# Kernel tuning notes

Hardware: AMD Instinct MI355X
Metric: run time of the kernel (lower is better)

## Reference

```python
import jax, jax.numpy as jnp
import numpy as np

B, S, D, H, HD = 1, 2048, 3072, 24, 128
FFN = int(D / 3 * 8)  # 8192
ADALN = 256
NORM_EPS = 1e-6
QK_EPS = 1e-5
AXES_DIMS = (16, 56, 56)
AXES_LENS = (64, 128, 128)
THETA = 256.0


def rmsnorm(x, w, eps):
    var = jnp.mean(jnp.square(x), axis=-1, keepdims=True)
    return x * jax.lax.rsqrt(var + eps) * w


def apply_rope(x, cos, sin):
    # x: [B,S,H,HD]; cos/sin: [B,S,HD//2] (broadcast over heads, matching freqs_cis.unsqueeze(2))
    xr = x[..., 0::2]
    xi = x[..., 1::2]
    c = cos[:, :, None, :]
    s = sin[:, :, None, :]
    or_ = xr * c - xi * s
    oi_ = xr * s + xi * c
    return jnp.stack([or_, oi_], axis=-1).reshape(x.shape)


def rope_angles(ids):
    # ids: [B,S,3] int; returns angles [B,S,HD//2] concatenated per axis like RopeEmbedder
    parts = []
    for d, idx_axis in zip(AXES_DIMS, range(len(AXES_DIMS))):
        freqs = 1.0 / (THETA ** (jnp.arange(0, d, 2, dtype=jnp.float32) / d))  # [d/2]
        ang = ids[..., idx_axis].astype(jnp.float32)[..., None] * freqs  # [B,S,d/2]
        parts.append(ang)
    return jnp.concatenate(parts, axis=-1)  # [B,S,64]


def setup_inputs() -> dict:
    key = jax.random.key(0)
    ks = jax.random.split(key, 20)
    w = 0.02
    ids = jnp.concatenate([
        jax.random.randint(ks[15], (B, S, 1), 0, AXES_LENS[0]),
        jax.random.randint(ks[16], (B, S, 1), 0, AXES_LENS[1]),
        jax.random.randint(ks[17], (B, S, 1), 0, AXES_LENS[2]),
    ], axis=-1)
    return {
        "x": jax.random.normal(ks[0], (B, S, D), jnp.float32),
        "adaln_input": jax.random.normal(ks[1], (B, ADALN), jnp.float32),
        "attn_mask": jnp.ones((B, S), dtype=bool),
        "ids": ids,
        "attn_norm1_w": jnp.ones((D,), jnp.float32),
        "attn_norm2_w": jnp.ones((D,), jnp.float32),
        "ffn_norm1_w": jnp.ones((D,), jnp.float32),
        "ffn_norm2_w": jnp.ones((D,), jnp.float32),
        "norm_q_w": jnp.ones((HD,), jnp.float32),
        "norm_k_w": jnp.ones((HD,), jnp.float32),
        "wq": jax.random.normal(ks[2], (D, D), jnp.float32) * w,
        "wk": jax.random.normal(ks[3], (D, D), jnp.float32) * w,
        "wv": jax.random.normal(ks[4], (D, D), jnp.float32) * w,
        "wo": jax.random.normal(ks[5], (D, D), jnp.float32) * w,
        "w1": jax.random.normal(ks[6], (D, FFN), jnp.float32) * w,
        "w2": jax.random.normal(ks[7], (FFN, D), jnp.float32) * w,
        "w3": jax.random.normal(ks[8], (D, FFN), jnp.float32) * w,
        "adaln_w": jax.random.normal(ks[9], (ADALN, 4 * D), jnp.float32) * w,
        "adaln_b": jnp.zeros((4 * D,), jnp.float32),
    }


def block_forward(x, adaln_input, attn_mask, ids,
                  attn_norm1_w, attn_norm2_w, ffn_norm1_w, ffn_norm2_w,
                  norm_q_w, norm_k_w, wq, wk, wv, wo, w1, w2, w3,
                  adaln_w, adaln_b):
    ang = rope_angles(ids)
    cos, sin = jnp.cos(ang), jnp.sin(ang)

    mod = adaln_input @ adaln_w + adaln_b
    scale_msa, gate_msa, scale_mlp, gate_mlp = jnp.split(mod[:, None, :], 4, axis=2)
    gate_msa, gate_mlp = jnp.tanh(gate_msa), jnp.tanh(gate_mlp)
    scale_msa, scale_mlp = 1.0 + scale_msa, 1.0 + scale_mlp

    # Attention branch
    xs = rmsnorm(x, attn_norm1_w, NORM_EPS) * scale_msa  # [B,S,D]
    q = (xs @ wq).reshape(B, S, H, HD)
    k = (xs @ wk).reshape(B, S, H, HD)
    v = (xs @ wv).reshape(B, S, H, HD)
    q = rmsnorm(q, norm_q_w, QK_EPS)
    k = rmsnorm(k, norm_k_w, QK_EPS)
    q = apply_rope(q, cos, sin)
    k = apply_rope(k, cos, sin)

    scores = jnp.einsum('bqhd,bkhd->bhqk', q, k) / jnp.sqrt(jnp.float32(HD))
    neg = jnp.finfo(scores.dtype).min
    scores = jnp.where(attn_mask[:, None, None, :], scores, neg)
    probs = jax.nn.softmax(scores, axis=-1)
    attn = jnp.einsum('bhqk,bkhd->bqhd', probs, v).reshape(B, S, D)
    attn_out = attn @ wo

    x = x + gate_msa * rmsnorm(attn_out, attn_norm2_w, NORM_EPS)

    # FFN branch (SwiGLU)
    xf = rmsnorm(x, ffn_norm1_w, NORM_EPS) * scale_mlp
    h = jax.nn.silu(xf @ w1) * (xf @ w3)
    ffn_out = h @ w2
    x = x + gate_mlp * rmsnorm(ffn_out, ffn_norm2_w, NORM_EPS)
    return x


def reference(x, adaln_input, attn_mask, ids,
              attn_norm1_w, attn_norm2_w, ffn_norm1_w, ffn_norm2_w,
              norm_q_w, norm_k_w, wq, wk, wv, wo, w1, w2, w3,
              adaln_w, adaln_b):
    return block_forward(x, adaln_input, attn_mask, ids,
                         attn_norm1_w, attn_norm2_w, ffn_norm1_w, ffn_norm2_w,
                         norm_q_w, norm_k_w, wq, wk, wv, wo, w1, w2, w3,
                         adaln_w, adaln_b)
```

## Files before the change

### kernel.cpp

```cpp
#include <hip/hip_runtime.h>

#define AS1 __attribute__((address_space(1)))
#define AS3 __attribute__((address_space(3)))

typedef __bf16 bf16;
using bf16x8 = __attribute__((ext_vector_type(8))) __bf16;
using bf16x4 = __attribute__((ext_vector_type(4))) __bf16;
using bf16x2 = __attribute__((ext_vector_type(2))) __bf16;
using f32x4  = __attribute__((ext_vector_type(4))) float;


__device__ inline float wsum(float v) {
#pragma unroll
  for (int o = 32; o; o >>= 1) v += __shfl_xor(v, o, 64);
  return v;
}

template <int EPI>
__global__ __launch_bounds__(512, 1) void gemm256(
    const bf16* __restrict__ A, const bf16* __restrict__ Bt, void* __restrict__ Cv,
    int K, int lda, int ldb, int ldc, long long kOff, long long sC) {
  __shared__ bf16 lds[2][2][256 * 64];
  const int t = threadIdx.x;
  const int lane = t & 63, wid = t >> 6;
  const int wm = wid >> 2, wn = wid & 3;
  const int row16 = lane & 15, kg = lane >> 4;
  const int m0 = blockIdx.x * 256, n0 = blockIdx.y * 256;
  const int NT = K >> 6;
  const int sgran = (lane & 7) ^ (lane >> 3);
  A += (long long)blockIdx.z * kOff;
  Bt += (long long)blockIdx.z * kOff;

  auto stageA = [&](int buf, int r, int tk) {
    const int wrow = ((wid & 4) << 5) + (r << 5) + ((wid & 3) << 3);
    __builtin_amdgcn_global_load_lds(
        (const AS1 void*)(A + (long long)(m0 + wrow + (lane >> 3)) * lda + tk * 64 +
                          (sgran << 3)),
        (AS3 void*)&lds[buf][0][wrow * 64], 16, 0, 0);
  };
  auto stageB = [&](int buf, int r, int tk) {
    const int wrow = ((wid & 4) << 5) + (r << 5) + ((wid & 3) << 3);
    __builtin_amdgcn_global_load_lds(
        (const AS1 void*)(Bt + (long long)(n0 + wrow + (lane >> 3)) * ldb + tk * 64 +
                          (sgran << 3)),
        (AS3 void*)&lds[buf][1][wrow * 64], 16, 0, 0);
  };

  f32x4 acc[8][4];
#pragma unroll
  for (int i = 0; i < 8; ++i)
#pragma unroll
    for (int j = 0; j < 4; ++j) acc[i][j] = (f32x4){0.f, 0.f, 0.f, 0.f};

#pragma unroll
  for (int r = 0; r < 4; ++r) { stageA(0, r, 0); stageB(0, r, 0); }
#pragma unroll
  for (int r = 0; r < 3; ++r) { stageA(1, r, 1); stageB(1, r, 1); }

  bf16x8 bfr[4][2], af[2][2];

  for (int kt = 0; kt < NT; ++kt) {
    const int cb = kt & 1, nb = cb ^ 1;
    if (kt + 1 < NT) asm volatile("s_waitcnt vmcnt(6)" ::: "memory");
    else             asm volatile("s_waitcnt vmcnt(0)" ::: "memory");
    __builtin_amdgcn_s_barrier();

    if (kt + 1 < NT) { stageA(nb, 3, kt + 1); stageB(nb, 3, kt + 1); }
#pragma unroll
    for (int ni = 0; ni < 4; ++ni)
#pragma unroll
      for (int kk = 0; kk < 2; ++kk) {
        const int r = wn * 64 + ni * 16 + row16;
        bfr[ni][kk] = *(const bf16x8*)&lds[cb][1][r * 64 + (((kk * 4 + kg) ^ (r & 7)) << 3)];
      }
#pragma unroll
    for (int mi = 0; mi < 2; ++mi)
#pragma unroll
      for (int kk = 0; kk < 2; ++kk) {
        const int r = wm * 128 + mi * 16 + row16;
        af[mi][kk] = *(const bf16x8*)&lds[cb][0][r * 64 + (((kk * 4 + kg) ^ (r & 7)) << 3)];
      }
    __builtin_amdgcn_s_barrier();
    asm volatile("s_waitcnt lgkmcnt(0)" ::: "memory");
    __builtin_amdgcn_s_setprio(1);
#pragma unroll
    for (int kk = 0; kk < 2; ++kk)
#pragma unroll
      for (int mi = 0; mi < 2; ++mi)
#pragma unroll
        for (int ni = 0; ni < 4; ++ni)
          acc[mi][ni] =
              __builtin_amdgcn_mfma_f32_16x16x32_bf16(af[mi][kk], bfr[ni][kk], acc[mi][ni], 0, 0, 0);
    __builtin_amdgcn_s_setprio(0);

#pragma unroll
    for (int q = 1; q < 4; ++q) {
      __builtin_amdgcn_s_barrier();
      if (kt + 2 < NT) { stageA(cb, q - 1, kt + 2); stageB(cb, q - 1, kt + 2); }
#pragma unroll
      for (int mi = 0; mi < 2; ++mi)
#pragma unroll
        for (int kk = 0; kk < 2; ++kk) {
          const int r = wm * 128 + q * 32 + mi * 16 + row16;
          af[mi][kk] = *(const bf16x8*)&lds[cb][0][r * 64 + (((kk * 4 + kg) ^ (r & 7)) << 3)];
        }
      __builtin_amdgcn_s_barrier();
      asm volatile("s_waitcnt lgkmcnt(0)" ::: "memory");
      __builtin_amdgcn_s_setprio(1);
#pragma unroll
      for (int kk = 0; kk < 2; ++kk)
#pragma unroll
        for (int mi = 0; mi < 2; ++mi)
#pragma unroll
          for (int ni = 0; ni < 4; ++ni)
            acc[q * 2 + mi][ni] = __builtin_amdgcn_mfma_f32_16x16x32_bf16(
                af[mi][kk], bfr[ni][kk], acc[q * 2 + mi][ni], 0, 0, 0);
      __builtin_amdgcn_s_setprio(0);
    }
  }

  float* Cf = (float*)Cv;
  bf16* Cb = (bf16*)Cv;
  const long long cz = (long long)blockIdx.z * sC;
#pragma unroll
  for (int mf = 0; mf < 8; ++mf)
#pragma unroll
    for (int ni = 0; ni < 4; ++ni)
#pragma unroll
      for (int rr = 0; rr < 4; ++rr) {
        const int row = m0 + wm * 128 + (mf >> 1) * 32 + (mf & 1) * 16 + kg * 4 + rr;
        const int col = n0 + wn * 64 + ni * 16 + row16;
        const long long idx = cz + (long long)row * ldc + col;
        const float v = acc[mf][ni][rr];
        if constexpr (EPI == 0) Cf[idx] = v;
        else Cb[idx] = (bf16)v;
      }
}

__global__ __launch_bounds__(256) void flash_attn_k(const bf16* __restrict__ qkv,
                                                    const bf16* __restrict__ vt,
                                                    float* __restrict__ Op,
                                                    float* __restrict__ mlp) {
  __shared__ bf16 Ks[64 * 128];
  __shared__ bf16 Vs[128 * 64];
  __shared__ bf16 Ps[4 * 32 * 64];
  const int t = threadIdx.x, lane = t & 63, wid = t >> 6;
  const int row16 = lane & 15, kg = lane >> 4;
  const int q0 = blockIdx.x * 128;
  const int h = blockIdx.y;
  const int z = blockIdx.z;
  const bf16* Qp = qkv + h * 128;
  const bf16* Kp = qkv + 3072 + h * 128;
  const bf16* Vt = vt + (long long)h * 262144;
  const float iscale = 0.08838834764831845f;

  bf16x8 qf[2][4];
#pragma unroll
  for (int mi = 0; mi < 2; ++mi)
#pragma unroll
    for (int kc = 0; kc < 4; ++kc)
      qf[mi][kc] = *(const bf16x8*)&Qp[(long long)(q0 + wid * 32 + mi * 16 + row16) * 9216 +
                                       kc * 32 + kg * 8];
  bf16x8 ones;
#pragma unroll
  for (int j = 0; j < 8; ++j) ones[j] = (bf16)1.0f;

  f32x4 oacc[2][8];
#pragma unroll
  for (int mi = 0; mi < 2; ++mi)
#pragma unroll
    for (int nd = 0; nd < 8; ++nd) oacc[mi][nd] = (f32x4){0.f, 0.f, 0.f, 0.f};
  f32x4 lacc[2] = {(f32x4){0.f, 0.f, 0.f, 0.f}, (f32x4){0.f, 0.f, 0.f, 0.f}};
  float mst[2][4];
#pragma unroll
  for (int mi = 0; mi < 2; ++mi)
#pragma unroll
    for (int r = 0; r < 4; ++r) mst[mi][r] = -1e30f;

  bf16* Pw = &Ps[wid * 2048];
  const int kvbase = z << 10;

  for (int kv0 = kvbase; kv0 < kvbase + 1024; kv0 += 64) {
#pragma unroll
    for (int p = 0; p < 4; ++p) {
      const int gi = p * 256 + t;
      const int row = gi >> 4, g = gi & 15;
      __builtin_amdgcn_global_load_lds(
          (const AS1 void*)(Kp + (long long)(kv0 + row) * 9216 + ((g ^ (row & 7)) << 3)),
          (AS3 void*)&Ks[(p * 256 + wid * 64) * 8], 16, 0, 0);
    }
#pragma unroll
    for (int p = 0; p < 4; ++p) {
      const int gi = p * 256 + t;
      const int row = gi >> 3, g = gi & 7;
      __builtin_amdgcn_global_load_lds(
          (const AS1 void*)(Vt + (long long)row * 2048 + kv0 + ((g ^ (row & 7)) << 3)),
          (AS3 void*)&Vs[(p * 256 + wid * 64) * 8], 16, 0, 0);
    }
    __syncthreads();

    f32x4 sacc[2][4];
#pragma unroll
    for (int mi = 0; mi < 2; ++mi)
#pragma unroll
      for (int nf = 0; nf < 4; ++nf) sacc[mi][nf] = (f32x4){0.f, 0.f, 0.f, 0.f};
#pragma unroll
    for (int kc = 0; kc < 4; ++kc) {
      bf16x8 kf[4];
#pragma unroll
      for (int nf = 0; nf < 4; ++nf) {
        const int row = nf * 16 + row16;
        kf[nf] = *(const bf16x8*)&Ks[(row * 16 + ((kc * 4 + kg) ^ (row & 7))) * 8];
      }
#pragma unroll
      for (int mi = 0; mi < 2; ++mi)
#pragma unroll
        for (int nf = 0; nf < 4; ++nf)
          sacc[mi][nf] =
              __builtin_amdgcn_mfma_f32_16x16x32_bf16(qf[mi][kc], kf[nf], sacc[mi][nf], 0, 0, 0);
    }

    float fac[2][4];
#pragma unroll
    for (int mi = 0; mi < 2; ++mi)
#pragma unroll
      for (int r = 0; r < 4; ++r) {
        float rm = sacc[mi][0][r];
#pragma unroll
        for (int nf = 1; nf < 4; ++nf) rm = fmaxf(rm, sacc[mi][nf][r]);
        rm = fmaxf(rm, __shfl_xor(rm, 1, 64));
        rm = fmaxf(rm, __shfl_xor(rm, 2, 64));
        rm = fmaxf(rm, __shfl_xor(rm, 4, 64));
        rm = fmaxf(rm, __shfl_xor(rm, 8, 64));
        const float mnew = fmaxf(mst[mi][r], rm * iscale);
        fac[mi][r] = __expf(mst[mi][r] - mnew);
        mst[mi][r] = mnew;
#pragma unroll
        for (int nf = 0; nf < 4; ++nf)
          sacc[mi][nf][r] = __expf(sacc[mi][nf][r] * iscale - mnew);
      }
#pragma unroll
    for (int mi = 0; mi < 2; ++mi)
#pragma unroll
      for (int r = 0; r < 4; ++r) {
        lacc[mi][r] *= fac[mi][r];
#pragma unroll
        for (int nd = 0; nd < 8; ++nd) oacc[mi][nd][r] *= fac[mi][r];
      }

#pragma unroll
    for (int mi = 0; mi < 2; ++mi)
#pragma unroll
      for (int nf = 0; nf < 4; ++nf)
#pragma unroll
        for (int r = 0; r < 4; ++r) {
          const int row = mi * 16 + kg * 4 + r;
          const int col = nf * 16 + row16;
          Pw[(row * 8 + ((col >> 3) ^ (row & 7))) * 8 + (col & 7)] = (bf16)sacc[mi][nf][r];
        }

#pragma unroll
    for (int kvc = 0; kvc < 2; ++kvc) {
      bf16x8 pf[2], vf[8];
#pragma unroll
      for (int mi = 0; mi < 2; ++mi) {
        const int row = mi * 16 + row16;
        pf[mi] = *(const bf16x8*)&Pw[(row * 8 + ((kvc * 4 + kg) ^ (row & 7))) * 8];
      }
#pragma unroll
      for (int nd = 0; nd < 8; ++nd) {
        const int row = nd * 16 + row16;
        vf[nd] = *(const bf16x8*)&Vs[(row * 8 + ((kvc * 4 + kg) ^ (row & 7))) * 8];
      }
#pragma unroll
      for (int mi = 0; mi < 2; ++mi) {
        lacc[mi] = __builtin_amdgcn_mfma_f32_16x16x32_bf16(pf[mi], ones, lacc[mi], 0, 0, 0);
#pragma unroll
        for (int nd = 0; nd < 8; ++nd)
          oacc[mi][nd] =
              __builtin_amdgcn_mfma_f32_16x16x32_bf16(pf[mi], vf[nd], oacc[mi][nd], 0, 0, 0);
      }
    }
    __syncthreads();
  }

  float* Oz = Op + (long long)z * 6291456;
#pragma unroll
  for (int mi = 0; mi < 2; ++mi)
#pragma unroll
    for (int nd = 0; nd < 8; ++nd)
#pragma unroll
      for (int r = 0; r < 4; ++r) {
        const int row = q0 + wid * 32 + mi * 16 + kg * 4 + r;
        const int col = h * 128 + nd * 16 + row16;
        Oz[(long long)row * 3072 + col] = oacc[mi][nd][r];
      }
  if (row16 == 0) {
#pragma unroll
    for (int mi = 0; mi < 2; ++mi)
#pragma unroll
      for (int r = 0; r < 4; ++r) {
        const int s = q0 + wid * 32 + mi * 16 + kg * 4 + r;
        const long long mi2 = ((long long)z * 49152 + s * 24 + h) * 2;
        mlp[mi2] = mst[mi][r];
        mlp[mi2 + 1] = lacc[mi][r];
      }
  }
}

__global__ __launch_bounds__(256) void fa_combine_k(const float* __restrict__ Op,
                                                    const float* __restrict__ mlp,
                                                    bf16* __restrict__ attn) {
  const int t = threadIdx.x, lane = t & 63, wid = t >> 6;
  const int pair = blockIdx.x * 4 + wid;
  const int s = pair / 24, h = pair % 24;
  const float2 ml0 = *(const float2*)&mlp[(long long)pair * 2];
  const float2 ml1 = *(const float2*)&mlp[(49152LL + pair) * 2];
  const float m = fmaxf(ml0.x, ml1.x);
  const float a0 = __expf(ml0.x - m), a1 = __expf(ml1.x - m);
  const float inv = 1.f / (ml0.y * a0 + ml1.y * a1);
  const long long base = (long long)s * 3072 + h * 128 + lane * 2;
  const float2 o0 = *(const float2*)&Op[base];
  const float2 o1 = *(const float2*)&Op[6291456LL + base];
  bf16x2 o;
  o[0] = (bf16)((o0.x * a0 + o1.x * a1) * inv);
  o[1] = (bf16)((o0.y * a0 + o1.y * a1) * inv);
  *(bf16x2*)&attn[base] = o;
}

__device__ inline void convT_tile(const float* __restrict__ in, bf16* __restrict__ out,
                                  int R, int C, int bx, int by) {
  __shared__ float tile[64][65];
  const int t = threadIdx.x;
  const int r0 = by * 64, c0 = bx * 64;
#pragma unroll
  for (int it = 0; it < 4; ++it) {
    const int idx = it * 256 + t;
    const int rl = idx >> 4, c4 = (idx & 15) << 2;
    const float4 v = *(const float4*)&in[(long long)(r0 + rl) * C + c0 + c4];
    tile[rl][c4 + 0] = v.x;
    tile[rl][c4 + 1] = v.y;
    tile[rl][c4 + 2] = v.z;
    tile[rl][c4 + 3] = v.w;
  }
  __syncthreads();
#pragma unroll
  for (int it = 0; it < 4; ++it) {
    const int idx = it * 256 + t;
    const int cl = idx >> 4, r4 = (idx & 15) << 2;
    bf16x4 o;
    o[0] = (bf16)tile[r4 + 0][cl];
    o[1] = (bf16)tile[r4 + 1][cl];
    o[2] = (bf16)tile[r4 + 2][cl];
    o[3] = (bf16)tile[r4 + 3][cl];
    *(bf16x4*)&out[(long long)(c0 + cl) * R + r0 + r4] = o;
  }
}

__global__ __launch_bounds__(256) void convAll(
    const float* __restrict__ wq, const float* __restrict__ wk,
    const float* __restrict__ wv, const float* __restrict__ wo,
    const float* __restrict__ w1, const float* __restrict__ w3,
    const float* __restrict__ w2, bf16* __restrict__ wqkvT, bf16* __restrict__ woT,
    bf16* __restrict__ w13T, bf16* __restrict__ w2T) {
  const int id = blockIdx.x;
  if (id < 9216) {
    const int m = id / 2304, l = id % 2304;
    const float* in = m == 0 ? wq : m == 1 ? wk : m == 2 ? wv : wo;
    bf16* out = m < 3 ? wqkvT + (long long)m * 9437184 : woT;
    convT_tile(in, out, 3072, 3072, l % 48, l / 48);
  } else if (id < 21504) {
    int l = id - 9216;
    const int m = l / 6144;
    l %= 6144;
    convT_tile(m ? w3 : w1, w13T + (long long)m * 25165824, 3072, 8192, l % 128, l / 128);
  } else {
    const int l = id - 21504;
    convT_tile(w2, w2T, 8192, 3072, l % 48, l / 48);
  }
}

__global__ __launch_bounds__(256) void ropetab_k(const int* __restrict__ ids,
                                                 float* __restrict__ cosT,
                                                 float* __restrict__ sinT) {
  const int i = blockIdx.x * 256 + threadIdx.x;
  const int s = i >> 6, j = i & 63;
  int ax, fi;
  float d;
  if (j < 8) { ax = 0; fi = j; d = 16.f; }
  else if (j < 36) { ax = 1; fi = j - 8; d = 56.f; }
  else { ax = 2; fi = j - 36; d = 56.f; }
  const float freq = exp2f(-16.f * (float)fi / d);
  const float ang = (float)ids[s * 3 + ax] * freq;
  cosT[i] = cosf(ang);
  sinT[i] = sinf(ang);
}

__global__ __launch_bounds__(256) void adaln_kernel(const float* __restrict__ ain,
                                                    const float* __restrict__ W,
                                                    const float* __restrict__ b,
                                                    float* __restrict__ out) {
  __shared__ float a[256];
  const int t = threadIdx.x;
  a[t] = ain[t];
  __syncthreads();
  const int n = blockIdx.x * 256 + t;
  float acc = b[n];
  for (int k = 0; k < 256; ++k) acc = fmaf(a[k], W[(long long)k * 12288 + n], acc);
  const int chunk = n / 3072;
  out[n] = (chunk & 1) ? tanhf(acc) : (1.f + acc);
}

__global__ __launch_bounds__(256) void rmsnorm_scale_k(const float* __restrict__ x,
                                                       const float* __restrict__ w,
                                                       const float* __restrict__ scale,
                                                       bf16* __restrict__ out) {
  __shared__ float red[4];
  const int t = threadIdx.x, lane = t & 63, wid = t >> 6;
  const long long base = (long long)blockIdx.x * 3072;
  float v[12];
  float ss = 0.f;
#pragma unroll
  for (int ch = 0; ch < 3; ++ch) {
    const float4 f = *(const float4*)&x[base + ch * 1024 + t * 4];
    v[ch * 4 + 0] = f.x; v[ch * 4 + 1] = f.y; v[ch * 4 + 2] = f.z; v[ch * 4 + 3] = f.w;
    ss += f.x * f.x + f.y * f.y + f.z * f.z + f.w * f.w;
  }
  ss = wsum(ss);
  if (!lane) red[wid] = ss;
  __syncthreads();
  const float r = rsqrtf((red[0] + red[1] + red[2] + red[3]) / 3072.f + 1e-6f);
#pragma unroll
  for (int ch = 0; ch < 3; ++ch) {
    const int col = ch * 1024 + t * 4;
    bf16x4 o;
#pragma unroll
    for (int j = 0; j < 4; ++j) o[j] = (bf16)(v[ch * 4 + j] * r * w[col + j] * scale[col + j]);
    *(bf16x4*)&out[base + col] = o;
  }
}

__global__ __launch_bounds__(256) void qknorm_rope_k(bf16* __restrict__ qkv,
                                                     const float* __restrict__ cosT,
                                                     const float* __restrict__ sinT,
                                                     const float* __restrict__ wq,
                                                     const float* __restrict__ wk) {
  const int t = threadIdx.x, lane = t & 63, wid = t >> 6;
  const int idx = blockIdx.x * 4 + wid;
  const int s = idx / 24, h = idx % 24;
  const int isK = blockIdx.y;
  bf16* base = qkv + (long long)s * 9216 + isK * 3072 + h * 128;
  bf16x2 p = *(const bf16x2*)(base + 2 * lane);
  float xr = (float)p[0], xi = (float)p[1];
  const float ss = wsum(xr * xr + xi * xi);
  const float r = rsqrtf(ss / 128.f + 1e-5f);
  const float* w = isK ? wk : wq;
  const float2 wv = *(const float2*)&w[2 * lane];
  xr *= r * wv.x;
  xi *= r * wv.y;
  const float c = cosT[s * 64 + lane], sn = sinT[s * 64 + lane];
  bf16x2 o;
  o[0] = (bf16)(xr * c - xi * sn);
  o[1] = (bf16)(xr * sn + xi * c);
  *(bf16x2*)(base + 2 * lane) = o;
}

__global__ __launch_bounds__(256) void vtrans_k(const bf16* __restrict__ qkv,
                                                bf16* __restrict__ vt) {
  __shared__ bf16 tile[64][72];
  const int t = threadIdx.x;
  const int s0 = blockIdx.x * 64, d0 = blockIdx.y * 64, h = blockIdx.z;
#pragma unroll
  for (int it = 0; it < 2; ++it) {
    const int idx = it * 256 + t;
    const int sl = idx >> 3, c8 = (idx & 7) << 3;
    const bf16x8 v =
        *(const bf16x8*)&qkv[(long long)(s0 + sl) * 9216 + 6144 + h * 128 + d0 + c8];
    *(bf16x8*)&tile[sl][c8] = v;
  }
  __syncthreads();
#pragma unroll
  for (int it = 0; it < 2; ++it) {
    const int idx = it * 256 + t;
    const int dl = idx >> 3, s8 = (idx & 7) << 3;
    bf16x8 o;
#pragma unroll
    for (int j = 0; j < 8; ++j) o[j] = tile[s8 + j][dl];
    *(bf16x8*)&vt[(long long)h * 262144 + (long long)(d0 + dl) * 2048 + s0 + s8] = o;
  }
}

__global__ __launch_bounds__(256) void silumul_k(const bf16* __restrict__ t13,
                                                 bf16* __restrict__ h) {
  const int gi = blockIdx.x * 256 + threadIdx.x;
  const int s = gi >> 10, j8 = (gi & 1023) << 3;
  const bf16x8 a = *(const bf16x8*)&t13[(long long)s * 16384 + j8];
  const bf16x8 b = *(const bf16x8*)&t13[(long long)s * 16384 + 8192 + j8];
  bf16x8 o;
#pragma unroll
  for (int j = 0; j < 8; ++j) {
    const float x = (float)a[j];
    const float sl = x / (1.f + __expf(-x));
    o[j] = (bf16)(sl * (float)b[j]);
  }
  *(bf16x8*)&h[(long long)s * 8192 + j8] = o;
}

__global__ __launch_bounds__(256) void resid1_k(
    const float* __restrict__ x, const float* __restrict__ p0, const float* __restrict__ p1,
    const float* __restrict__ n2w, const float* __restrict__ gate,
    const float* __restrict__ f1w, const float* __restrict__ smlp,
    float* __restrict__ x1, bf16* __restrict__ xf) {
  __shared__ float red[8];
  const int t = threadIdx.x, lane = t & 63, wid = t >> 6;
  const long long base = (long long)blockIdx.x * 3072;
  float av[12];
  float ss = 0.f;
#pragma unroll
  for (int ch = 0; ch < 3; ++ch) {
    const float4 f0 = *(const float4*)&p0[base + ch * 1024 + t * 4];
    const float4 f1 = *(const float4*)&p1[base + ch * 1024 + t * 4];
    const float a0 = f0.x + f1.x, a1 = f0.y + f1.y, a2 = f0.z + f1.z, a3 = f0.w + f1.w;
    av[ch * 4 + 0] = a0; av[ch * 4 + 1] = a1; av[ch * 4 + 2] = a2; av[ch * 4 + 3] = a3;
    ss += a0 * a0 + a1 * a1 + a2 * a2 + a3 * a3;
  }
  ss = wsum(ss);
  if (!lane) red[wid] = ss;
  __syncthreads();
  const float r = rsqrtf((red[0] + red[1] + red[2] + red[3]) / 3072.f + 1e-6f);
  float xv[12];
  float ss2 = 0.f;
#pragma unroll
  for (int ch = 0; ch < 3; ++ch) {
    const int col = ch * 1024 + t * 4;
    const float4 f = *(const float4*)&x[base + col];
    float4 o;
    o.x = f.x + gate[col + 0] * (av[ch * 4 + 0] * r * n2w[col + 0]);
    o.y = f.y + gate[col + 1] * (av[ch * 4 + 1] * r * n2w[col + 1]);
    o.z = f.z + gate[col + 2] * (av[ch * 4 + 2] * r * n2w[col + 2]);
    o.w = f.w + gate[col + 3] * (av[ch * 4 + 3] * r * n2w[col + 3]);
    *(float4*)&x1[base + col] = o;
    xv[ch * 4 + 0] = o.x; xv[ch * 4 + 1] = o.y; xv[ch * 4 + 2] = o.z; xv[ch * 4 + 3] = o.w;
    ss2 += o.x * o.x + o.y * o.y + o.z * o.z + o.w * o.w;
  }
  ss2 = wsum(ss2);
  if (!lane) red[4 + wid] = ss2;
  __syncthreads();
  const float r2 = rsqrtf((red[4] + red[5] + red[6] + red[7]) / 3072.f + 1e-6f);
#pragma unroll
  for (int ch = 0; ch < 3; ++ch) {
    const int col = ch * 1024 + t * 4;
    bf16x4 o;
#pragma unroll
    for (int j = 0; j < 4; ++j)
      o[j] = (bf16)(xv[ch * 4 + j] * r2 * f1w[col + j] * smlp[col + j]);
    *(bf16x4*)&xf[base + col] = o;
  }
}

__global__ __launch_bounds__(256) void resid2_k(const float* __restrict__ x1,
                                                const float* __restrict__ f0,
                                                const float* __restrict__ f1,
                                                const float* __restrict__ nw,
                                                const float* __restrict__ gate,
                                                float* __restrict__ out) {
  __shared__ float red[4];
  const int t = threadIdx.x, lane = t & 63, wid = t >> 6;
  const long long base = (long long)blockIdx.x * 3072;
  float fv[12];
  float ss = 0.f;
#pragma unroll
  for (int ch = 0; ch < 3; ++ch) {
    const float4 a = *(const float4*)&f0[base + ch * 1024 + t * 4];
    const float4 b = *(const float4*)&f1[base + ch * 1024 + t * 4];
    const float a0 = a.x + b.x, a1 = a.y + b.y, a2 = a.z + b.z, a3 = a.w + b.w;
    fv[ch * 4 + 0] = a0; fv[ch * 4 + 1] = a1; fv[ch * 4 + 2] = a2; fv[ch * 4 + 3] = a3;
    ss += a0 * a0 + a1 * a1 + a2 * a2 + a3 * a3;
  }
  ss = wsum(ss);
  if (!lane) red[wid] = ss;
  __syncthreads();
  const float r = rsqrtf((red[0] + red[1] + red[2] + red[3]) / 3072.f + 1e-6f);
#pragma unroll
  for (int ch = 0; ch < 3; ++ch) {
    const int col = ch * 1024 + t * 4;
    const float4 f = *(const float4*)&x1[base + col];
    float4 o;
    o.x = f.x + gate[col + 0] * (fv[ch * 4 + 0] * r * nw[col + 0]);
    o.y = f.y + gate[col + 1] * (fv[ch * 4 + 1] * r * nw[col + 1]);
    o.z = f.z + gate[col + 2] * (fv[ch * 4 + 2] * r * nw[col + 2]);
    o.w = f.w + gate[col + 3] * (fv[ch * 4 + 3] * r * nw[col + 3]);
    *(float4*)&out[base + col] = o;
  }
}

extern "C" void kernel_launch(void* const* d_in, const int* in_sizes, int n_in,
                              void* d_out, int out_size, void* d_ws, size_t ws_size,
                              hipStream_t stream) {
  const float* x    = (const float*)d_in[0];
  const float* ain  = (const float*)d_in[1];
  const int* ids    = (const int*)d_in[3];
  const float* n1w  = (const float*)d_in[4];
  const float* n2w  = (const float*)d_in[5];
  const float* fn1w = (const float*)d_in[6];
  const float* fn2w = (const float*)d_in[7];
  const float* nqw  = (const float*)d_in[8];
  const float* nkw  = (const float*)d_in[9];
  const float* wq   = (const float*)d_in[10];
  const float* wk   = (const float*)d_in[11];
  const float* wv   = (const float*)d_in[12];
  const float* wo   = (const float*)d_in[13];
  const float* w1   = (const float*)d_in[14];
  const float* w2   = (const float*)d_in[15];
  const float* w3   = (const float*)d_in[16];
  const float* adw  = (const float*)d_in[17];
  const float* adb  = (const float*)d_in[18];

  if (ws_size < 395362304ULL) return;

  char* ws = (char*)d_ws;
  bf16* wqkvT = (bf16*)(ws + 0LL);
  bf16* woT   = (bf16*)(ws + 56623104LL);
  bf16* w13T  = (bf16*)(ws + 75497472LL);
  bf16* w2T   = (bf16*)(ws + 176160768LL);
  float* cosT = (float*)(ws + 226492416LL);
  float* sinT = (float*)(ws + 227016704LL);
  float* adv  = (float*)(ws + 227540992LL);
  bf16* xs    = (bf16*)(ws + 227590144LL);
  char* big   = ws + 240173056LL;
  float* x1   = (float*)(big);
  bf16* qkv   = (bf16*)(big + 25165824LL);
  bf16* vt    = (bf16*)(big + 62914560LL);
  bf16* attn  = (bf16*)(big + 75497472LL);
  float* aoP  = (float*)(big + 88080384LL);
  float* Opart= (float*)(big + 88080384LL);
  float* mlp  = (float*)(big + 138412032LL);
  bf16* t13   = (bf16*)(big + 25165824LL);
  bf16* hbuf  = (bf16*)(big + 92274688LL);
  float* ffnP = (float*)(big + 25165824LL);

  const dim3 b256(256);
  const dim3 b512(512);

  ropetab_k<<<dim3(512), b256, 0, stream>>>(ids, cosT, sinT);
  adaln_kernel<<<dim3(48), b256, 0, stream>>>(ain, adw, adb, adv);

  convAll<<<dim3(27648), b256, 0, stream>>>(wq, wk, wv, wo, w1, w3, w2, wqkvT, woT, w13T,
                                            w2T);

  rmsnorm_scale_k<<<dim3(2048), b256, 0, stream>>>(x, n1w, adv, xs);

  gemm256<1><<<dim3(8, 36, 1), b512, 0, stream>>>(xs, wqkvT, qkv, 3072, 3072, 3072, 9216,
                                                  0LL, 0LL);

  qknorm_rope_k<<<dim3(12288, 2), b256, 0, stream>>>(qkv, cosT, sinT, nqw, nkw);
  vtrans_k<<<dim3(32, 2, 24), b256, 0, stream>>>(qkv, vt);

  flash_attn_k<<<dim3(16, 24, 2), b256, 0, stream>>>(qkv, vt, Opart, mlp);
  fa_combine_k<<<dim3(12288), b256, 0, stream>>>(Opart, mlp, attn);

  gemm256<0><<<dim3(8, 12, 2), b512, 0, stream>>>(attn, woT, aoP, 1536, 3072, 3072, 3072,
                                                  1536LL, 6291456LL);
  resid1_k<<<dim3(2048), b256, 0, stream>>>(x, aoP, aoP + 6291456LL, n2w, adv + 3072, fn1w,
                                            adv + 6144, x1, xs);
  gemm256<1><<<dim3(8, 64, 1), b512, 0, stream>>>(xs, w13T, t13, 3072, 3072, 3072, 16384,
                                                  0LL, 0LL);
  silumul_k<<<dim3(8192), b256, 0, stream>>>(t13, hbuf);
  gemm256<0><<<dim3(8, 12, 2), b512, 0, stream>>>(hbuf, w2T, ffnP, 4096, 8192, 8192, 3072,
                                                  4096LL, 6291456LL);
  resid2_k<<<dim3(2048), b256, 0, stream>>>(x1, ffnP, ffnP + 6291456LL, fn2w, adv + 9216,
                                            (float*)d_out);
}
```

Measured before the change: 886.1 us.

## Template GEMM on N-tile width and use 256x192 tiles for QKV, Wo, W2

Parameterizes the bf16 GEMM kernel on the number of 16-wide N fragments per wave, splitting LDS into separate A and B buffers and adapting the B staging pattern for 192-wide tiles. The QKV, output-projection and W2 GEMMs switch to 256x192 tiles so their grids (384 and 256 blocks) map onto the CU count better than the old 288- and 192-block grids with 256x256 tiles. The secondary barrier after each LDS fragment read is also removed to cut synchronization. The trade-off is lower arithmetic intensity per tile and more global traffic for B, plus some risk from the relaxed barrier schedule.

```diff
diff --git a/kernel.cpp b/kernel.cpp
--- a/kernel.cpp
+++ b/kernel.cpp
@@ -16,16 +16,19 @@
   return v;
 }
 
-template <int EPI>
+template <int EPI, int NI>
 __global__ __launch_bounds__(512, 1) void gemm256(
     const bf16* __restrict__ A, const bf16* __restrict__ Bt, void* __restrict__ Cv,
     int K, int lda, int ldb, int ldc, long long kOff, long long sC) {
-  __shared__ bf16 lds[2][2][256 * 64];
+  constexpr int BN = NI * 64;
+  constexpr int BROUNDS = (NI == 4) ? 4 : 3;
+  __shared__ bf16 ldsA[2][256 * 64];
+  __shared__ bf16 ldsB[2][BN * 64];
   const int t = threadIdx.x;
   const int lane = t & 63, wid = t >> 6;
   const int wm = wid >> 2, wn = wid & 3;
   const int row16 = lane & 15, kg = lane >> 4;
-  const int m0 = blockIdx.x * 256, n0 = blockIdx.y * 256;
+  const int m0 = blockIdx.x * 256, n0 = blockIdx.y * BN;
   const int NT = K >> 6;
   const int sgran = (lane & 7) ^ (lane >> 3);
   A += (long long)blockIdx.z * kOff;
@@ -36,28 +39,32 @@
     __builtin_amdgcn_global_load_lds(
         (const AS1 void*)(A + (long long)(m0 + wrow + (lane >> 3)) * lda + tk * 64 +
                           (sgran << 3)),
-        (AS3 void*)&lds[buf][0][wrow * 64], 16, 0, 0);
+        (AS3 void*)&ldsA[buf][wrow * 64], 16, 0, 0);
   };
   auto stageB = [&](int buf, int r, int tk) {
-    const int wrow = ((wid & 4) << 5) + (r << 5) + ((wid & 3) << 3);
+    int wrow;
+    if constexpr (NI == 4) wrow = ((wid & 4) << 5) + (r << 5) + ((wid & 3) << 3);
+    else                   wrow = r * 64 + wid * 8;
     __builtin_amdgcn_global_load_lds(
         (const AS1 void*)(Bt + (long long)(n0 + wrow + (lane >> 3)) * ldb + tk * 64 +
                           (sgran << 3)),
-        (AS3 void*)&lds[buf][1][wrow * 64], 16, 0, 0);
+        (AS3 void*)&ldsB[buf][wrow * 64], 16, 0, 0);
   };
 
-  f32x4 acc[8][4];
+  f32x4 acc[8][NI];
 #pragma unroll
   for (int i = 0; i < 8; ++i)
 #pragma unroll
-    for (int j = 0; j < 4; ++j) acc[i][j] = (f32x4){0.f, 0.f, 0.f, 0.f};
-
-#pragma unroll
-  for (int r = 0; r < 4; ++r) { stageA(0, r, 0); stageB(0, r, 0); }
+    for (int j = 0; j < NI; ++j) acc[i][j] = (f32x4){0.f, 0.f, 0.f, 0.f};
+
+#pragma unroll
+  for (int r = 0; r < 4; ++r) stageA(0, r, 0);
+#pragma unroll
+  for (int r = 0; r < BROUNDS; ++r) stageB(0, r, 0);
 #pragma unroll
   for (int r = 0; r < 3; ++r) { stageA(1, r, 1); stageB(1, r, 1); }
 
-  bf16x8 bfr[4][2], af[2][2];
+  bf16x8 bfr[NI][2], af[2][2];
 
   for (int kt = 0; kt < NT; ++kt) {
     const int cb = kt & 1, nb = cb ^ 1;
@@ -65,22 +72,24 @@
     else             asm volatile("s_waitcnt vmcnt(0)" ::: "memory");
     __builtin_amdgcn_s_barrier();
 
-    if (kt + 1 < NT) { stageA(nb, 3, kt + 1); stageB(nb, 3, kt + 1); }
-#pragma unroll
-    for (int ni = 0; ni < 4; ++ni)
+    if (kt + 1 < NT) {
+      stageA(nb, 3, kt + 1);
+      if constexpr (NI == 4) stageB(nb, 3, kt + 1);
+    }
+#pragma unroll
+    for (int ni = 0; ni < NI; ++ni)
 #pragma unroll
       for (int kk = 0; kk < 2; ++kk) {
-        const int r = wn * 64 + ni * 16 + row16;
-        bfr[ni][kk] = *(const bf16x8*)&lds[cb][1][r * 64 + (((kk * 4 + kg) ^ (r & 7)) << 3)];
+        const int r = wn * (16 * NI) + ni * 16 + row16;
+        bfr[ni][kk] = *(const bf16x8*)&ldsB[cb][r * 64 + (((kk * 4 + kg) ^ (r & 7)) << 3)];
       }
 #pragma unroll
     for (int mi = 0; mi < 2; ++mi)
 #pragma unroll
       for (int kk = 0; kk < 2; ++kk) {
         const int r = wm * 128 + mi * 16 + row16;
-        af[mi][kk] = *(const bf16x8*)&lds[cb][0][r * 64 + (((kk * 4 + kg) ^ (r & 7)) << 3)];
-      }
-    __builtin_amdgcn_s_barrier();
+        af[mi][kk] = *(const bf16x8*)&ldsA[cb][r * 64 + (((kk * 4 + kg) ^ (r & 7)) << 3)];
+      }
     asm volatile("s_waitcnt lgkmcnt(0)" ::: "memory");
     __builtin_amdgcn_s_setprio(1);
 #pragma unroll
@@ -88,7 +97,7 @@
 #pragma unroll
       for (int mi = 0; mi < 2; ++mi)
 #pragma unroll
-        for (int ni = 0; ni < 4; ++ni)
+        for (int ni = 0; ni < NI; ++ni)
           acc[mi][ni] =
               __builtin_amdgcn_mfma_f32_16x16x32_bf16(af[mi][kk], bfr[ni][kk], acc[mi][ni], 0, 0, 0);
     __builtin_amdgcn_s_setprio(0);
@@ -102,9 +111,8 @@
 #pragma unroll
         for (int kk = 0; kk < 2; ++kk) {
           const int r = wm * 128 + q * 32 + mi * 16 + row16;
-          af[mi][kk] = *(const bf16x8*)&lds[cb][0][r * 64 + (((kk * 4 + kg) ^ (r & 7)) << 3)];
+          af[mi][kk] = *(const bf16x8*)&ldsA[cb][r * 64 + (((kk * 4 + kg) ^ (r & 7)) << 3)];
         }
-      __builtin_amdgcn_s_barrier();
       asm volatile("s_waitcnt lgkmcnt(0)" ::: "memory");
       __builtin_amdgcn_s_setprio(1);
 #pragma unroll
@@ -112,7 +120,7 @@
 #pragma unroll
         for (int mi = 0; mi < 2; ++mi)
 #pragma unroll
-          for (int ni = 0; ni < 4; ++ni)
+          for (int ni = 0; ni < NI; ++ni)
             acc[q * 2 + mi][ni] = __builtin_amdgcn_mfma_f32_16x16x32_bf16(
                 af[mi][kk], bfr[ni][kk], acc[q * 2 + mi][ni], 0, 0, 0);
       __builtin_amdgcn_s_setprio(0);
@@ -125,11 +133,11 @@
 #pragma unroll
   for (int mf = 0; mf < 8; ++mf)
 #pragma unroll
-    for (int ni = 0; ni < 4; ++ni)
+    for (int ni = 0; ni < NI; ++ni)
 #pragma unroll
       for (int rr = 0; rr < 4; ++rr) {
         const int row = m0 + wm * 128 + (mf >> 1) * 32 + (mf & 1) * 16 + kg * 4 + rr;
-        const int col = n0 + wn * 64 + ni * 16 + row16;
+        const int col = n0 + wn * (16 * NI) + ni * 16 + row16;
         const long long idx = cz + (long long)row * ldc + col;
         const float v = acc[mf][ni][rr];
         if constexpr (EPI == 0) Cf[idx] = v;
@@ -650,8 +658,8 @@
 
   rmsnorm_scale_k<<<dim3(2048), b256, 0, stream>>>(x, n1w, adv, xs);
 
-  gemm256<1><<<dim3(8, 36, 1), b512, 0, stream>>>(xs, wqkvT, qkv, 3072, 3072, 3072, 9216,
-                                                  0LL, 0LL);
+  gemm256<1, 3><<<dim3(8, 48, 1), b512, 0, stream>>>(xs, wqkvT, qkv, 3072, 3072, 3072,
+                                                     9216, 0LL, 0LL);
 
   qknorm_rope_k<<<dim3(12288, 2), b256, 0, stream>>>(qkv, cosT, sinT, nqw, nkw);
   vtrans_k<<<dim3(32, 2, 24), b256, 0, stream>>>(qkv, vt);
@@ -659,15 +667,15 @@
   flash_attn_k<<<dim3(16, 24, 2), b256, 0, stream>>>(qkv, vt, Opart, mlp);
   fa_combine_k<<<dim3(12288), b256, 0, stream>>>(Opart, mlp, attn);
 
-  gemm256<0><<<dim3(8, 12, 2), b512, 0, stream>>>(attn, woT, aoP, 1536, 3072, 3072, 3072,
-                                                  1536LL, 6291456LL);
+  gemm256<0, 3><<<dim3(8, 16, 2), b512, 0, stream>>>(attn, woT, aoP, 1536, 3072, 3072,
+                                                     3072, 1536LL, 6291456LL);
   resid1_k<<<dim3(2048), b256, 0, stream>>>(x, aoP, aoP + 6291456LL, n2w, adv + 3072, fn1w,
                                             adv + 6144, x1, xs);
-  gemm256<1><<<dim3(8, 64, 1), b512, 0, stream>>>(xs, w13T, t13, 3072, 3072, 3072, 16384,
-                                                  0LL, 0LL);
+  gemm256<1, 4><<<dim3(8, 64, 1), b512, 0, stream>>>(xs, w13T, t13, 3072, 3072, 3072,
+                                                     16384, 0LL, 0LL);
   silumul_k<<<dim3(8192), b256, 0, stream>>>(t13, hbuf);
-  gemm256<0><<<dim3(8, 12, 2), b512, 0, stream>>>(hbuf, w2T, ffnP, 4096, 8192, 8192, 3072,
-                                                  4096LL, 6291456LL);
+  gemm256<0, 3><<<dim3(8, 16, 2), b512, 0, stream>>>(hbuf, w2T, ffnP, 4096, 8192, 8192,
+                                                     3072, 4096LL, 6291456LL);
   resid2_k<<<dim3(2048), b256, 0, stream>>>(x1, ffnP, ffnP + 6291456LL, fn2w, adv + 9216,
                                             (float*)d_out);
 }
```

Measured after the change: 1.300 ms. 1.47x slower.
